# Kernel tuning notes

Measured on AMD Instinct MI355X. Metric: run time of the kernel, lower is better.

Reference implementation:

```python
import jax, jax.numpy as jnp
import numpy as np

K = 8192          # num_embeddings
D = 256           # embedding_dim
DECAY = 0.95
EPS = 1e-05
COMMIT = 0.25


def setup_inputs() -> dict:
    key = jax.random.key(0)
    k1, k2, k3 = jax.random.split(key, 3)
    x = jax.random.normal(k1, (32, D, 32, 32), dtype=jnp.float32)
    codebook = jax.random.uniform(k2, (K, D), dtype=jnp.float32,
                                  minval=-1.0 / K, maxval=1.0 / K)
    ema_count = jnp.zeros((K,), dtype=jnp.float32)
    ema_weight = jax.random.normal(k3, (K, D), dtype=jnp.float32)
    return {"x": x, "codebook": codebook, "ema_count": ema_count,
            "ema_weight": ema_weight}


def reference(x, codebook, ema_count, ema_weight):
    b, c, h, w = x.shape
    inputs = jnp.transpose(x, (0, 2, 3, 1))          # [B,H,W,C]
    flat = inputs.reshape(-1, c)                     # [N,C], N=B*H*W
    n = flat.shape[0]

    # squared euclidean distances: ||z||^2 + ||e||^2 - 2 z.e
    distances = (jnp.sum(flat * flat, axis=1, keepdims=True)
                 + jnp.sum(codebook * codebook, axis=1)
                 - 2.0 * flat @ codebook.T)          # [N,K]
    idx = jnp.argmin(distances, axis=1)              # [N]

    # one-hot @ codebook == gather
    quantized = codebook[idx].reshape(inputs.shape)  # [B,H,W,C]

    # EMA codebook update (training branch, no-grad in torch)
    counts = jax.ops.segment_sum(jnp.ones((n,), flat.dtype), idx,
                                 num_segments=K)     # encodings.sum(0)
    new_count = ema_count * DECAY + (1.0 - DECAY) * counts
    new_count = (new_count + EPS) / (n + K * EPS) * n
    dw = jax.ops.segment_sum(flat, idx, num_segments=K)  # encodings.T @ flat
    new_weight = ema_weight * DECAY + (1.0 - DECAY) * dw
    new_codebook = new_weight / new_count[:, None]

    e_loss = COMMIT * jnp.mean((jax.lax.stop_gradient(quantized) - inputs) ** 2)
    quantized_st = inputs + jax.lax.stop_gradient(quantized - inputs)

    indices = idx.reshape(b, h * w)
    return (e_loss,
            jnp.transpose(quantized_st, (0, 3, 1, 2)),
            indices,
            new_count, new_weight, new_codebook)
```

## Files before the change

### kernel.cpp

```cpp
#include <hip/hip_runtime.h>
#include <stdint.h>

#define N_TOK 32768
#define DIM   256
#define KCB   8192
#define HWSZ  1024

#define WS_FLATB   0u
#define WS_CBB     4194304u
#define WS_A32     5242880u
#define WS_B32     5275648u
#define WS_IDX     5283840u
#define WS_CAND    5316608u
#define WS_ICNT    5840896u
#define WS_CUR     5849088u
#define WS_OFFS    5857280u
#define WS_PERM    5865472u
#define WS_LPART   5898240u
#define WS_DW      5914624u
#define WS_TOTAL   8011776u
#define WS_MEMSET_LEN 16384u

#define O_LOSS 0u
#define O_Q    1u
#define O_IDX  8388609u
#define O_CNT  8421377u
#define O_W    8429569u
#define O_CB   10526721u

typedef __attribute__((ext_vector_type(8))) short bf16x8;
typedef __attribute__((ext_vector_type(4))) float f32x4;

__device__ __forceinline__ void g2lds16(const void* gp, void* lp){
  __builtin_amdgcn_global_load_lds(
      (const __attribute__((address_space(1))) void*)gp,
      (__attribute__((address_space(3))) void*)lp, 16, 0, 0);
}

__device__ __forceinline__ unsigned short f2b(float f){
  unsigned u = __float_as_uint(f);
  return (unsigned short)((u + 0x7FFFu + ((u >> 16) & 1u)) >> 16);
}

__device__ __forceinline__ unsigned umin2(unsigned a, unsigned b){ return a < b ? a : b; }
__device__ __forceinline__ unsigned umax2(unsigned a, unsigned b){ return a > b ? a : b; }

__device__ __forceinline__ float np_pairwise_sq(const float* __restrict__ p, int stride){
  #pragma clang fp contract(off)
  float h[2];
  #pragma unroll
  for (int half = 0; half < 2; half++){
    const float* q = p + half * 128 * stride;
    float r[8];
    #pragma unroll
    for (int j = 0; j < 8; j++){ float z = q[j * stride]; r[j] = z * z; }
    for (int i = 8; i < 128; i += 8){
      #pragma unroll
      for (int j = 0; j < 8; j++){ float z = q[(i + j) * stride]; r[j] = r[j] + z * z; }
    }
    h[half] = ((r[0] + r[1]) + (r[2] + r[3])) + ((r[4] + r[5]) + (r[6] + r[7]));
  }
  return h[0] + h[1];
}

__global__ void k_prep(const float* __restrict__ x, const float* __restrict__ cb,
                       unsigned short* __restrict__ flatB, unsigned short* __restrict__ cbB,
                       float* __restrict__ a32, float* __restrict__ b32)
{
  __shared__ float tile[64][65];
  const int bx = blockIdx.x;
  const int t = threadIdx.x;
  if (bx < 2048){
    const int b = bx >> 6, ct = (bx >> 4) & 3, ht = bx & 15;
    const int c0 = ct * 64, hw0 = ht * 64;
    const int rr = t >> 4, cc4 = (t & 15) * 4;
    #pragma unroll
    for (int j = 0; j < 4; j++){
      const int crow = rr + j * 16;
      float4 v = *(const float4*)(x + ((size_t)(b * 256 + c0 + crow) << 10) + hw0 + cc4);
      tile[crow][cc4] = v.x; tile[crow][cc4+1] = v.y; tile[crow][cc4+2] = v.z; tile[crow][cc4+3] = v.w;
    }
    __syncthreads();
    #pragma unroll
    for (int j = 0; j < 4; j++){
      const int hwrow = rr + j * 16;
      ushort4 o = { f2b(tile[cc4][hwrow]), f2b(tile[cc4+1][hwrow]),
                    f2b(tile[cc4+2][hwrow]), f2b(tile[cc4+3][hwrow]) };
      *(ushort4*)(flatB + ((size_t)(b * 1024 + hw0 + hwrow) << 8) + c0 + cc4) = o;
    }
  } else if (bx < 4096){
    const int g = (bx - 2048) * 256 + t;
    float4 v = *(const float4*)(cb + (size_t)g * 4);
    ushort4 o = { f2b(v.x), f2b(v.y), f2b(v.z), f2b(v.w) };
    *(ushort4*)(cbB + (size_t)g * 4) = o;
  } else {
    const int g = (bx - 4096) * 256 + t;
    if (g < N_TOK){
      int b = g >> 10, hw = g & 1023;
      a32[g] = np_pairwise_sq(x + (size_t)b * 262144 + hw, 1024);
    } else {
      int k2 = g - N_TOK;
      b32[k2] = np_pairwise_sq(cb + (size_t)k2 * 256, 1);
    }
  }
}

__launch_bounds__(256, 2)
__global__ void k_dist(const unsigned short* __restrict__ flatB,
                       const unsigned short* __restrict__ cbB,
                       const float* __restrict__ b32,
                       int* __restrict__ cand)
{
  __shared__ __align__(16) unsigned short A1[128 * 128];
  __shared__ __align__(16) unsigned short Bs[2][128 * 64];

  const int tid = threadIdx.x;
  const int bx = blockIdx.x;
  const int tt = bx >> 1, h = bx & 1;
  const int tok0 = tt * 128;
  const int wv = tid >> 6, lane = tid & 63;
  const int wy = wv >> 1, wx = wv & 1;
  const int l4 = lane >> 4, lm = lane & 15;

  const unsigned short* fB = flatB + (size_t)tok0 * 256;
  const unsigned short* cB = cbB + (size_t)h * 4096 * 256;

  {
    const int r = lane >> 4, p = lane & 15;
    #pragma unroll
    for (int j = 0; j < 8; j++){
      const int row = wv * 32 + j * 4 + r;
      const int gc = p ^ (row & 15);
      g2lds16((const char*)fB + (size_t)row * 512 + (gc << 4),
              (char*)A1 + (wv * 32 + j * 4) * 256);
    }
    unsigned short* A2 = &Bs[0][0];
    #pragma unroll
    for (int j = 0; j < 8; j++){
      const int row = wv * 32 + j * 4 + r;
      const int gc = p ^ (row & 15);
      g2lds16((const char*)fB + (size_t)row * 512 + 256 + (gc << 4),
              (char*)A2 + (wv * 32 + j * 4) * 256);
    }
  }
  __syncthreads();

  bf16x8 a2[4][4];
  {
    const unsigned short* A2 = &Bs[0][0];
    #pragma unroll
    for (int ks4 = 0; ks4 < 4; ks4++)
      #pragma unroll
      for (int ii = 0; ii < 4; ii++){
        const int m = wy * 64 + ii * 16 + lm;
        const int c = ks4 * 4 + l4;
        a2[ks4][ii] = *(const bf16x8*)((const char*)A2 + m * 256 + ((c ^ (m & 15)) << 4));
      }
  }
  __syncthreads();

  unsigned aoff[4][4];
  #pragma unroll
  for (int kg = 0; kg < 4; kg++)
    #pragma unroll
    for (int ii = 0; ii < 4; ii++){
      const int m = wy * 64 + ii * 16 + lm;
      const int ca = kg * 4 + l4;
      aoff[kg][ii] = (unsigned)(m * 256 + ((ca ^ (m & 15)) << 4));
    }
  unsigned boff[2][2][4];
  #pragma unroll
  for (int buf = 0; buf < 2; buf++)
    #pragma unroll
    for (int ks2 = 0; ks2 < 2; ks2++)
      #pragma unroll
      for (int jj = 0; jj < 4; jj++){
        const int n = wx * 64 + jj * 16 + lm;
        const int c2 = ks2 * 4 + l4;
        boff[buf][ks2][jj] = (unsigned)(buf * 16384 + n * 128 + ((c2 ^ (n & 7)) << 4));
      }
  const char* gBj[4];
  unsigned dstj[4];
  {
    const int r8 = lane >> 3, p = lane & 7;
    #pragma unroll
    for (int j = 0; j < 4; j++){
      const int row = wv * 32 + j * 8 + r8;
      const int gc = p ^ (row & 7);
      gBj[j] = (const char*)cB + (size_t)row * 512 + (gc << 4);
      dstj[j] = (unsigned)((wv * 32 + j * 8) * 128);
    }
  }

  auto stageB = [&](int S2){
    const int ss = S2 & 3, cc = S2 >> 2;
    const int buf = (S2 & 1) * 16384;
    const size_t soff = (size_t)(cc * 65536 + ss * 128);
    #pragma unroll
    for (int j = 0; j < 4; j++)
      g2lds16(gBj[j] + soff, (char*)Bs + buf + dstj[j]);
  };

  unsigned k1[16], k2[16];
  #pragma unroll
  for (int i = 0; i < 16; i++){ k1[i] = 0xFFFFFFFFu; k2[i] = 0xFFFFFFFFu; }

  f32x4 acc[4][4];
  float bn125[4];

  stageB(0);
  __syncthreads();

  for (int c = 0; c < 32; c++){
    #pragma unroll
    for (int s = 0; s < 4; s++){
      const int S = c * 4 + s;
      if (S + 1 < 128) stageB(S + 1);
      if (s == 0){
        #pragma unroll
        for (int jj = 0; jj < 4; jj++)
          bn125[jj] = b32[h * 4096 + c * 128 + wx * 64 + jj * 16 + lm] + 0.125f;
        #pragma unroll
        for (int ii = 0; ii < 4; ii++)
          #pragma unroll
          for (int jj = 0; jj < 4; jj++)
            acc[ii][jj] = (f32x4){0.f, 0.f, 0.f, 0.f};
      }
      #pragma unroll
      for (int ks2 = 0; ks2 < 2; ks2++){
        const int kg = s * 2 + ks2;
        bf16x8 bf[4], af[4];
        #pragma unroll
        for (int jj = 0; jj < 4; jj++)
          bf[jj] = *(const bf16x8*)((const char*)Bs + boff[s & 1][ks2][jj]);
        if (kg < 4){
          #pragma unroll
          for (int ii = 0; ii < 4; ii++)
            af[ii] = *(const bf16x8*)((const char*)A1 + aoff[kg][ii]);
        } else {
          #pragma unroll
          for (int ii = 0; ii < 4; ii++) af[ii] = a2[kg - 4][ii];
        }
        #pragma unroll
        for (int ii = 0; ii < 4; ii++)
          #pragma unroll
          for (int jj = 0; jj < 4; jj++)
            acc[ii][jj] = __builtin_amdgcn_mfma_f32_16x16x32_bf16(af[ii], bf[jj], acc[ii][jj], 0, 0, 0);
      }
      if (s == 3){
        unsigned pk[4];
        #pragma unroll
        for (int jj = 0; jj < 4; jj++) pk[jj] = (unsigned)((c << 2) | jj);
        #pragma unroll
        for (int ii = 0; ii < 4; ii++){
          #pragma unroll
          for (int r = 0; r < 4; r++){
            const int rk = ii * 4 + r;
            unsigned kb[4];
            #pragma unroll
            for (int jj = 0; jj < 4; jj++){
              const float v = fmaf(-2.f, acc[ii][jj][r], bn125[jj]);
              kb[jj] = (__float_as_uint(v) & 0xFFFFFF80u) | pk[jj];
            }
            const unsigned lo01 = umin2(kb[0], kb[1]), hi01 = umax2(kb[0], kb[1]);
            const unsigned lo23 = umin2(kb[2], kb[3]), hi23 = umax2(kb[2], kb[3]);
            const unsigned s1 = umin2(lo01, lo23);
            const unsigned s2 = umin2(umax2(lo01, lo23), umin2(hi01, hi23));
            const unsigned t = umax2(k1[rk], s1);
            k1[rk] = umin2(k1[rk], s1);
            k2[rk] = umin2(umin2(k2[rk], t), s2);
          }
        }
      }
      __syncthreads();
    }
  }

  const unsigned colbase = (unsigned)(wx * 64 + lm);
  auto fin = [colbase](unsigned key)->unsigned {
    const float v125 = __uint_as_float(key & 0xFFFFFF80u);
    int qi = (int)(v125 * 4194304.f);
    qi = qi < 0 ? 0 : (qi > 0xFFFFF ? 0xFFFFF : qi);
    const unsigned cc = (key >> 2) & 31u, jj = key & 3u;
    return ((unsigned)qi << 12) | (cc * 128u + jj * 16u + colbase);
  };
  unsigned* red = (unsigned*)&A1[0];
  #pragma unroll
  for (int rk = 0; rk < 16; rk++){
    const int srow = wy * 64 + (rk >> 2) * 16 + l4 * 4 + (rk & 3);
    red[srow * 64 + wx * 32 + lm * 2 + 0] = fin(k1[rk]);
    red[srow * 64 + wx * 32 + lm * 2 + 1] = fin(k2[rk]);
  }
  __syncthreads();
  if (tid < 128){
    unsigned best[8];
    #pragma unroll
    for (int j = 0; j < 8; j++) best[j] = 0xFFFFFFFFu;
    for (int i = 0; i < 64; i++){
      unsigned k = red[tid * 64 + i];
      if (k < best[7]){
        best[7] = k;
        #pragma unroll
        for (int j = 7; j > 0; j--){
          if (best[j] < best[j-1]){ unsigned tmp = best[j]; best[j] = best[j-1]; best[j-1] = tmp; }
        }
      }
    }
    const size_t base = ((size_t)(tok0 + tid) * 2 + h) * 8;
    #pragma unroll
    for (int j = 0; j < 8; j++) cand[base + j] = h * 4096 + (int)(best[j] & 0xFFFu);
  }
}

__global__ void k_pick(const float* __restrict__ x, const float* __restrict__ cb,
                       const float* __restrict__ a32, const float* __restrict__ b32,
                       const int* __restrict__ cand, int* __restrict__ idx,
                       int* __restrict__ icnt, float* __restrict__ out_idx)
{
  const int gt = blockIdx.x * 256 + threadIdx.x;
  const int wid = gt >> 6;
  const int lane = gt & 63;
  const int tq = lane & 3, cg = lane >> 2;
  const int n = wid * 4 + tq;
  const int b = n >> 10, hw = n & 1023;

  float z[16];
  {
    const float* xb = x + (((size_t)(b * 256 + cg * 16)) << 10) + hw;
    #pragma unroll
    for (int j = 0; j < 16; j++) z[j] = xb[(size_t)j << 10];
  }
  const float an = a32[n];
  float bestd = 3.4e38f; int besti = 0x7fffffff;
  for (int j = 0; j < 16; j++){
    const int ci = cand[(size_t)n * 16 + j];
    if (ci < 0 || ci >= KCB) continue;
    const float* ep = cb + (size_t)ci * DIM + cg * 16;
    float4 e0 = *(const float4*)(ep + 0);
    float4 e1 = *(const float4*)(ep + 4);
    float4 e2 = *(const float4*)(ep + 8);
    float4 e3 = *(const float4*)(ep + 12);
    double se = (double)z[0]*e0.x + (double)z[1]*e0.y + (double)z[2]*e0.z + (double)z[3]*e0.w
              + (double)z[4]*e1.x + (double)z[5]*e1.y + (double)z[6]*e1.z + (double)z[7]*e1.w
              + (double)z[8]*e2.x + (double)z[9]*e2.y + (double)z[10]*e2.z + (double)z[11]*e2.w
              + (double)z[12]*e3.x + (double)z[13]*e3.y + (double)z[14]*e3.z + (double)z[15]*e3.w;
    se += __shfl_xor(se, 4, 64);
    se += __shfl_xor(se, 8, 64);
    se += __shfl_xor(se, 16, 64);
    se += __shfl_xor(se, 32, 64);
    const float A = an + b32[ci];
    const float d32 = (float)((double)A - 2.0 * se);
    if (d32 < bestd || (d32 == bestd && ci < besti)){ bestd = d32; besti = ci; }
  }
  if (cg == 0){
    idx[n] = besti;
    atomicAdd(icnt + besti, 1);
    out_idx[n] = (float)besti;
  }
}

__global__ void k_perm(const int* __restrict__ idx, const int* __restrict__ icnt,
                       int* __restrict__ cur, int* __restrict__ perm,
                       int* __restrict__ offs)
{
  __shared__ int offs_l[8192];
  __shared__ int sums[256];
  const int tid = threadIdx.x;
  int loc[32];
  int s = 0;
  #pragma unroll
  for (int i = 0; i < 32; i++){ loc[i] = s; s += icnt[tid * 32 + i]; }
  sums[tid] = s;
  #pragma unroll
  for (int off = 1; off < 256; off <<= 1){
    __syncthreads();
    const int add = (tid >= off) ? sums[tid - off] : 0;
    __syncthreads();
    sums[tid] += add;
  }
  __syncthreads();
  const int pre = (tid == 0) ? 0 : sums[tid - 1];
  #pragma unroll
  for (int i = 0; i < 32; i++) offs_l[tid * 32 + i] = pre + loc[i];
  if (blockIdx.x == 0){
    #pragma unroll
    for (int i = 0; i < 32; i++) offs[tid * 32 + i] = pre + loc[i];
  }
  __syncthreads();
  const int t = blockIdx.x * 256 + tid;
  const int code = idx[t];
  const int slot = atomicAdd(cur + code, 1);
  perm[offs_l[code] + slot] = t;
}

__global__ void k_dw(const unsigned short* __restrict__ flatB,
                     const int* __restrict__ offs, const int* __restrict__ icnt,
                     const int* __restrict__ perm, float* __restrict__ dw)
{
  const int k = blockIdx.x;
  const int c = threadIdx.x;
  const int start = offs[k], cnt = icnt[k];
  float s = 0.f;
  for (int i = 0; i < cnt; i++){
    const int n = perm[start + i];
    s += __uint_as_float(((unsigned)flatB[((size_t)n << 8) + c]) << 16);
  }
  dw[((size_t)k << 8) + c] = s;
}

__global__ void k_quant(const float* __restrict__ x, const float* __restrict__ cb,
                        const int* __restrict__ idx, float* __restrict__ outq,
                        double* __restrict__ lpart)
{
  __shared__ float qt[64][65];
  __shared__ double wred[4];
  const int bx = blockIdx.x;
  const int tid = threadIdx.x;
  const int b = bx >> 6, ct = (bx >> 4) & 3, ht = bx & 15;
  const int c0 = ct * 64, hw0 = ht * 64;
  const int n0 = b * 1024 + hw0;

  {
    const int cl = tid & 63, wq = tid >> 6;
    for (int r16 = 0; r16 < 16; r16++){
      const int row = r16 * 4 + wq;
      const int i = idx[n0 + row];
      qt[row][cl] = cb[(size_t)i * DIM + c0 + cl];
    }
  }
  __syncthreads();

  const int cc = tid >> 4;
  const int hw4 = (tid & 15) * 4;
  double p = 0.0;
  #pragma unroll
  for (int j = 0; j < 4; j++){
    const int cl = cc + j * 16;
    const size_t xo = (((size_t)(b * 256 + c0 + cl)) << 10) + hw0 + hw4;
    float4 xv = *(const float4*)(x + xo);
    float q0 = qt[hw4 + 0][cl];
    float q1 = qt[hw4 + 1][cl];
    float q2 = qt[hw4 + 2][cl];
    float q3 = qt[hw4 + 3][cl];
    float qd0 = q0 - xv.x, qd1 = q1 - xv.y, qd2 = q2 - xv.z, qd3 = q3 - xv.w;
    float4 ov = { xv.x + qd0, xv.y + qd1, xv.z + qd2, xv.w + qd3 };
    *(float4*)(outq + xo) = ov;
    p += (double)(qd0*qd0 + qd1*qd1 + qd2*qd2 + qd3*qd3);
  }
  #pragma unroll
  for (int o = 32; o > 0; o >>= 1) p += __shfl_down(p, o, 64);
  if ((tid & 63) == 0) wred[tid >> 6] = p;
  __syncthreads();
  if (tid == 0) lpart[bx] = (wred[0] + wred[1]) + (wred[2] + wred[3]);
}

__global__ void k_final(const float* __restrict__ ema_w, const float* __restrict__ dw,
                        const int* __restrict__ icnt, const float* __restrict__ ema_count,
                        const double* __restrict__ lpart, float* __restrict__ out)
{
  const int k = blockIdx.x;
  const int tid = threadIdx.x;
  float ct1 = ema_count[k] * 0.95f;
  float ct2 = 0.05f * (float)icnt[k];
  float s  = ct1 + ct2;
  float s2 = s + 1e-5f;
  const float DEN = (float)(32768.0 + 8192.0 * 1e-5);
  float nc = (s2 / DEN) * 32768.0f;
  if (tid == 0) out[O_CNT + k] = nc;
  {
    #pragma clang fp contract(off)
    const int t = k * 256 + tid;
    float w = ema_w[t];
    float d = dw[t];
    float t1 = w * 0.95f;
    float t2 = 0.05f * d;
    float nw = t1 + t2;
    out[O_W + t]  = nw;
    out[O_CB + t] = nw / nc;
  }
  if (k == 0){
    __shared__ double sred[256];
    double ls = 0.0;
    for (int i = tid; i < 2048; i += 256) ls += lpart[i];
    sred[tid] = ls;
    __syncthreads();
    for (int off = 128; off > 0; off >>= 1){
      if (tid < off) sred[tid] += sred[tid + off];
      __syncthreads();
    }
    if (tid == 0) out[O_LOSS] = 0.25f * (float)(sred[0] / 8388608.0);
  }
}

extern "C" void kernel_launch(void* const* d_in, const int* in_sizes, int n_in,
                              void* d_out, int out_size, void* d_ws, size_t ws_size,
                              hipStream_t stream)
{
  const float* x         = (const float*)d_in[0];
  const float* cb        = (const float*)d_in[1];
  const float* ema_count = (const float*)d_in[2];
  const float* ema_w     = (const float*)d_in[3];
  float* out = (float*)d_out;
  float* ws  = (float*)d_ws;

  unsigned short* flatB = (unsigned short*)(ws + WS_FLATB);
  unsigned short* cbB   = (unsigned short*)(ws + WS_CBB);
  float*  a32    = ws + WS_A32;
  float*  b32    = ws + WS_B32;
  int*    idxp   = (int*)(ws + WS_IDX);
  int*    candp  = (int*)(ws + WS_CAND);
  int*    icnt   = (int*)(ws + WS_ICNT);
  int*    curp   = (int*)(ws + WS_CUR);
  int*    offs   = (int*)(ws + WS_OFFS);
  int*    permp  = (int*)(ws + WS_PERM);
  double* lpart  = (double*)(ws + WS_LPART);
  float*  dwp    = ws + WS_DW;

  (void)hipMemsetAsync(ws + WS_ICNT, 0, (size_t)WS_MEMSET_LEN * sizeof(float), stream);

  k_prep <<<4256, 256, 0, stream>>>(x, cb, flatB, cbB, a32, b32);
  k_dist <<<512,  256, 0, stream>>>(flatB, cbB, b32, candp);
  k_pick <<<2048, 256, 0, stream>>>(x, cb, a32, b32, candp, idxp, icnt, out + O_IDX);
  k_perm <<<128,  256, 0, stream>>>(idxp, icnt, curp, permp, offs);
  k_dw   <<<8192, 256, 0, stream>>>(flatB, offs, icnt, permp, dwp);
  k_quant<<<2048, 256, 0, stream>>>(x, cb, idxp, out + O_Q, lpart);
  k_final<<<8192, 256, 0, stream>>>(ema_w, dwp, icnt, ema_count, lpart, out);
}
```

Baseline: 384.9 us.

## Fuse quantize/loss into pick kernel and dw accumulation into EMA final kernel

The quantized output and per-block loss partials are now computed inside k_pick, reusing the token values already held in registers and gathering the chosen codebook row directly. This removes the separate k_quant pass that re-read x and gathered codebook rows. The dw segment sum is also merged with the EMA count/weight/codebook update, so the intermediate dw buffer is no longer written and re-read and two launches are dropped. The trade-off is that k_pick's output stores are strided across channels (1 KB apart per element) instead of coalesced float4 tiles.

```diff
diff --git a/kernel.cpp b/kernel.cpp
--- a/kernel.cpp
+++ b/kernel.cpp
@@ -315,8 +315,10 @@
 __global__ void k_pick(const float* __restrict__ x, const float* __restrict__ cb,
                        const float* __restrict__ a32, const float* __restrict__ b32,
                        const int* __restrict__ cand, int* __restrict__ idx,
-                       int* __restrict__ icnt, float* __restrict__ out_idx)
-{
+                       int* __restrict__ icnt, float* __restrict__ out_idx,
+                       float* __restrict__ outq, double* __restrict__ lpart)
+{
+  __shared__ double wred[4];
   const int gt = blockIdx.x * 256 + threadIdx.x;
   const int wid = gt >> 6;
   const int lane = gt & 63;
@@ -324,12 +326,11 @@
   const int n = wid * 4 + tq;
   const int b = n >> 10, hw = n & 1023;
 
+  const size_t xbase = (((size_t)(b * 256 + cg * 16)) << 10) + hw;
   float z[16];
-  {
-    const float* xb = x + (((size_t)(b * 256 + cg * 16)) << 10) + hw;
-    #pragma unroll
-    for (int j = 0; j < 16; j++) z[j] = xb[(size_t)j << 10];
-  }
+  #pragma unroll
+  for (int j = 0; j < 16; j++) z[j] = x[xbase + ((size_t)j << 10)];
+
   const float an = a32[n];
   float bestd = 3.4e38f; int besti = 0x7fffffff;
   for (int j = 0; j < 16; j++){
@@ -352,11 +353,34 @@
     const float d32 = (float)((double)A - 2.0 * se);
     if (d32 < bestd || (d32 == bestd && ci < besti)){ bestd = d32; besti = ci; }
   }
+
+  double p = 0.0;
+  {
+    const float* ep = cb + (size_t)besti * DIM + cg * 16;
+    float4 e0 = *(const float4*)(ep + 0);
+    float4 e1 = *(const float4*)(ep + 4);
+    float4 e2 = *(const float4*)(ep + 8);
+    float4 e3 = *(const float4*)(ep + 12);
+    float q[16] = { e0.x, e0.y, e0.z, e0.w, e1.x, e1.y, e1.z, e1.w,
+                    e2.x, e2.y, e2.z, e2.w, e3.x, e3.y, e3.z, e3.w };
+    #pragma unroll
+    for (int j = 0; j < 16; j++){
+      const float qd = q[j] - z[j];
+      outq[xbase + ((size_t)j << 10)] = z[j] + qd;
+      p += (double)(qd * qd);
+    }
+  }
+  #pragma unroll
+  for (int o = 32; o > 0; o >>= 1) p += __shfl_down(p, o, 64);
+  if ((threadIdx.x & 63) == 0) wred[threadIdx.x >> 6] = p;
+
   if (cg == 0){
     idx[n] = besti;
     atomicAdd(icnt + besti, 1);
     out_idx[n] = (float)besti;
   }
+  __syncthreads();
+  if (threadIdx.x == 0) lpart[blockIdx.x] = (wred[0] + wred[1]) + (wred[2] + wred[3]);
 }
 
 __global__ void k_perm(const int* __restrict__ idx, const int* __restrict__ icnt,
@@ -393,9 +417,11 @@
   perm[offs_l[code] + slot] = t;
 }
 
-__global__ void k_dw(const unsigned short* __restrict__ flatB,
-                     const int* __restrict__ offs, const int* __restrict__ icnt,
-                     const int* __restrict__ perm, float* __restrict__ dw)
+__global__ void k_dwf(const unsigned short* __restrict__ flatB,
+                      const int* __restrict__ offs, const int* __restrict__ icnt,
+                      const int* __restrict__ perm,
+                      const float* __restrict__ ema_w, const float* __restrict__ ema_count,
+                      const double* __restrict__ lpart, float* __restrict__ out)
 {
   const int k = blockIdx.x;
   const int c = threadIdx.x;
@@ -405,75 +431,19 @@
     const int n = perm[start + i];
     s += __uint_as_float(((unsigned)flatB[((size_t)n << 8) + c]) << 16);
   }
-  dw[((size_t)k << 8) + c] = s;
-}
-
-__global__ void k_quant(const float* __restrict__ x, const float* __restrict__ cb,
-                        const int* __restrict__ idx, float* __restrict__ outq,
-                        double* __restrict__ lpart)
-{
-  __shared__ float qt[64][65];
-  __shared__ double wred[4];
-  const int bx = blockIdx.x;
-  const int tid = threadIdx.x;
-  const int b = bx >> 6, ct = (bx >> 4) & 3, ht = bx & 15;
-  const int c0 = ct * 64, hw0 = ht * 64;
-  const int n0 = b * 1024 + hw0;
-
-  {
-    const int cl = tid & 63, wq = tid >> 6;
-    for (int r16 = 0; r16 < 16; r16++){
-      const int row = r16 * 4 + wq;
-      const int i = idx[n0 + row];
-      qt[row][cl] = cb[(size_t)i * DIM + c0 + cl];
-    }
-  }
-  __syncthreads();
-
-  const int cc = tid >> 4;
-  const int hw4 = (tid & 15) * 4;
-  double p = 0.0;
-  #pragma unroll
-  for (int j = 0; j < 4; j++){
-    const int cl = cc + j * 16;
-    const size_t xo = (((size_t)(b * 256 + c0 + cl)) << 10) + hw0 + hw4;
-    float4 xv = *(const float4*)(x + xo);
-    float q0 = qt[hw4 + 0][cl];
-    float q1 = qt[hw4 + 1][cl];
-    float q2 = qt[hw4 + 2][cl];
-    float q3 = qt[hw4 + 3][cl];
-    float qd0 = q0 - xv.x, qd1 = q1 - xv.y, qd2 = q2 - xv.z, qd3 = q3 - xv.w;
-    float4 ov = { xv.x + qd0, xv.y + qd1, xv.z + qd2, xv.w + qd3 };
-    *(float4*)(outq + xo) = ov;
-    p += (double)(qd0*qd0 + qd1*qd1 + qd2*qd2 + qd3*qd3);
-  }
-  #pragma unroll
-  for (int o = 32; o > 0; o >>= 1) p += __shfl_down(p, o, 64);
-  if ((tid & 63) == 0) wred[tid >> 6] = p;
-  __syncthreads();
-  if (tid == 0) lpart[bx] = (wred[0] + wred[1]) + (wred[2] + wred[3]);
-}
-
-__global__ void k_final(const float* __restrict__ ema_w, const float* __restrict__ dw,
-                        const int* __restrict__ icnt, const float* __restrict__ ema_count,
-                        const double* __restrict__ lpart, float* __restrict__ out)
-{
-  const int k = blockIdx.x;
-  const int tid = threadIdx.x;
   float ct1 = ema_count[k] * 0.95f;
-  float ct2 = 0.05f * (float)icnt[k];
-  float s  = ct1 + ct2;
-  float s2 = s + 1e-5f;
+  float ct2 = 0.05f * (float)cnt;
+  float sc  = ct1 + ct2;
+  float sc2 = sc + 1e-5f;
   const float DEN = (float)(32768.0 + 8192.0 * 1e-5);
-  float nc = (s2 / DEN) * 32768.0f;
-  if (tid == 0) out[O_CNT + k] = nc;
+  float nc = (sc2 / DEN) * 32768.0f;
+  if (c == 0) out[O_CNT + k] = nc;
   {
     #pragma clang fp contract(off)
-    const int t = k * 256 + tid;
+    const int t = k * 256 + c;
     float w = ema_w[t];
-    float d = dw[t];
     float t1 = w * 0.95f;
-    float t2 = 0.05f * d;
+    float t2 = 0.05f * s;
     float nw = t1 + t2;
     out[O_W + t]  = nw;
     out[O_CB + t] = nw / nc;
@@ -481,14 +451,14 @@
   if (k == 0){
     __shared__ double sred[256];
     double ls = 0.0;
-    for (int i = tid; i < 2048; i += 256) ls += lpart[i];
-    sred[tid] = ls;
+    for (int i = c; i < 2048; i += 256) ls += lpart[i];
+    sred[c] = ls;
     __syncthreads();
     for (int off = 128; off > 0; off >>= 1){
-      if (tid < off) sred[tid] += sred[tid + off];
+      if (c < off) sred[c] += sred[c + off];
       __syncthreads();
     }
-    if (tid == 0) out[O_LOSS] = 0.25f * (float)(sred[0] / 8388608.0);
+    if (c == 0) out[O_LOSS] = 0.25f * (float)(sred[0] / 8388608.0);
   }
 }
 
@@ -514,15 +484,14 @@
   int*    offs   = (int*)(ws + WS_OFFS);
   int*    permp  = (int*)(ws + WS_PERM);
   double* lpart  = (double*)(ws + WS_LPART);
-  float*  dwp    = ws + WS_DW;
 
   (void)hipMemsetAsync(ws + WS_ICNT, 0, (size_t)WS_MEMSET_LEN * sizeof(float), stream);
 
   k_prep <<<4256, 256, 0, stream>>>(x, cb, flatB, cbB, a32, b32);
   k_dist <<<512,  256, 0, stream>>>(flatB, cbB, b32, candp);
-  k_pick <<<2048, 256, 0, stream>>>(x, cb, a32, b32, candp, idxp, icnt, out + O_IDX);
+  k_pick <<<2048, 256, 0, stream>>>(x, cb, a32, b32, candp, idxp, icnt,
+                                    out + O_IDX, out + O_Q, lpart);
   k_perm <<<128,  256, 0, stream>>>(idxp, icnt, curp, permp, offs);
-  k_dw   <<<8192, 256, 0, stream>>>(flatB, offs, icnt, permp, dwp);
-  k_quant<<<2048, 256, 0, stream>>>(x, cb, idxp, out + O_Q, lpart);
-  k_final<<<8192, 256, 0, stream>>>(ema_w, dwp, icnt, ema_count, lpart, out);
-}
+  k_dwf  <<<8192, 256, 0, stream>>>(flatB, offs, icnt, permp, ema_w, ema_count,
+                                    lpart, out);
+}
```

Result: no change. 384.3 us (-0.1%).
